# Kernel optimization log

Measured on AMD Instinct MI355X. Metric: run time of the kernel, lower is better.

## Reference

```python
import jax, jax.numpy as jnp
import numpy as np

B = 32768
IN_DIM = 768
HIDDENS = [2048, 1024, 512]
EMBED_DIM = 128
NUM_EMB = 1024
DEPTH = 3


def setup_inputs() -> dict:
    key = jax.random.key(0)
    ks = jax.random.split(key, 20)
    d = {"x": jax.random.normal(ks[0], (B, IN_DIM), dtype=jnp.float32)}
    # Encoder: in -> h0 -> h1 -> h2 -> embed  (weights stored as [in, out])
    enc_dims = [IN_DIM] + HIDDENS + [EMBED_DIM]
    for i in range(4):
        fan_in = enc_dims[i]
        d[f"enc_W{i+1}"] = jax.random.normal(ks[1 + i], (enc_dims[i], enc_dims[i + 1]), dtype=jnp.float32) / np.sqrt(fan_in)
        d[f"enc_b{i+1}"] = jnp.zeros((enc_dims[i + 1],), dtype=jnp.float32)
    # Decoder: embed -> h0 -> h1 -> h2 -> in
    dec_dims = [EMBED_DIM] + HIDDENS + [IN_DIM]
    for i in range(4):
        fan_in = dec_dims[i]
        d[f"dec_W{i+1}"] = jax.random.normal(ks[5 + i], (dec_dims[i], dec_dims[i + 1]), dtype=jnp.float32) / np.sqrt(fan_in)
        d[f"dec_b{i+1}"] = jnp.zeros((dec_dims[i + 1],), dtype=jnp.float32)
    # Codebook (nn.Embedding weight, initialized ~ N(0,1) as in the module)
    d["codebook"] = jax.random.normal(ks[9], (NUM_EMB, EMBED_DIM), dtype=jnp.float32)
    return d


def _encoder(x, W1, b1, W2, b2, W3, b3, W4, b4):
    x = jax.nn.relu(x @ W1 + b1)
    x = jax.nn.relu(x @ W2 + b2)
    x = jax.nn.relu(x @ W3 + b3)
    return x @ W4 + b4


def _decoder(x, W1, b1, W2, b2, W3, b3, W4, b4):
    x = jax.nn.relu(x @ W1 + b1)
    x = jax.nn.relu(x @ W2 + b2)
    x = jax.nn.relu(x @ W3 + b3)
    return x @ W4 + b4


def reference(x,
              enc_W1, enc_b1, enc_W2, enc_b2, enc_W3, enc_b3, enc_W4, enc_b4,
              dec_W1, dec_b1, dec_W2, dec_b2, dec_W3, dec_b3, dec_W4, dec_b4,
              codebook):
    z = _encoder(x, enc_W1, enc_b1, enc_W2, enc_b2, enc_W3, enc_b3, enc_W4, enc_b4)
    z_det = jax.lax.stop_gradient(z)

    cb_sq = jnp.sum(codebook * codebook, axis=1)  # [K]
    residue = z_det
    z_hat = jnp.zeros_like(z_det)
    codes = []
    for _ in range(DEPTH):  # residual quantization loop
        # squared L2 distances [B, K]
        dist = (jnp.sum(residue * residue, axis=1, keepdims=True)
                + cb_sq
                - 2.0 * residue @ codebook.T)
        idx = jnp.argmin(dist, axis=1)          # [B]
        codes.append(idx)
        z_hat = z_hat + codebook[idx]           # gather codebook vectors
        residue = z_det - z_hat
    all_codes = jnp.stack(codes, axis=1)        # [B, DEPTH] int

    # straight-through estimator: forward uses z_hat, grad flows through z
    z_flow = z + jax.lax.stop_gradient(z_hat - z)
    x_recon = _decoder(z_flow, dec_W1, dec_b1, dec_W2, dec_b2, dec_W3, dec_b3, dec_W4, dec_b4)
    return (x_recon, all_codes)
```

## Files before the change

kernel.cpp:

```cpp
#include <hip/hip_runtime.h>

#define FLT_MAX_C 3.402823466e+38f

typedef __attribute__((ext_vector_type(8))) __bf16 bf16x8;
typedef __attribute__((ext_vector_type(4))) float f32x4;

static __device__ __forceinline__ ushort f2bf(float x) {
    union { float f; unsigned u; } v; v.f = x;
    unsigned r = (v.u + 0x7FFFu + ((v.u >> 16) & 1u)) >> 16;
    return (ushort)r;
}

template<bool RELU>
__global__ __launch_bounds__(256) void gemm_f32(
    const float* __restrict__ A, const float* __restrict__ W,
    const float* __restrict__ bias, float* __restrict__ C,
    int M, int K, int N)
{
    __shared__ float As[8][128];
    __shared__ float Bs[8][132];
    const int tid = threadIdx.x;
    const int bm = blockIdx.y << 7;
    const int bn = blockIdx.x << 7;

    const int la_row = tid >> 1;
    const int la_k   = (tid & 1) << 2;
    const int lb_row = tid >> 5;
    const int lb_col = (tid & 31) << 2;
    const int tm4 = (tid >> 4) << 2;
    const int tn4 = (tid & 15) << 2;

    float acc[8][8];
    #pragma unroll
    for (int i = 0; i < 8; ++i)
        #pragma unroll
        for (int j = 0; j < 8; ++j) acc[i][j] = 0.f;

    const float* aptr = A + (size_t)(bm + la_row) * K + la_k;
    const float* bptr = W + (size_t)lb_row * N + bn + lb_col;

    float4 av = *(const float4*)(aptr);
    float4 bv = *(const float4*)(bptr);

    for (int k0 = 0; k0 < K; k0 += 8) {
        __syncthreads();
        As[la_k + 0][la_row] = av.x;
        As[la_k + 1][la_row] = av.y;
        As[la_k + 2][la_row] = av.z;
        As[la_k + 3][la_row] = av.w;
        *(float4*)(&Bs[lb_row][lb_col]) = bv;
        __syncthreads();
        if (k0 + 8 < K) {
            av = *(const float4*)(aptr + k0 + 8);
            bv = *(const float4*)(bptr + (size_t)(k0 + 8) * N);
        }
        #pragma unroll
        for (int kk = 0; kk < 8; ++kk) {
            float a[8], b[8];
            *(float4*)(a)     = *(const float4*)(&As[kk][tm4]);
            *(float4*)(a + 4) = *(const float4*)(&As[kk][tm4 + 64]);
            *(float4*)(b)     = *(const float4*)(&Bs[kk][tn4]);
            *(float4*)(b + 4) = *(const float4*)(&Bs[kk][tn4 + 64]);
            #pragma unroll
            for (int i = 0; i < 8; ++i)
                #pragma unroll
                for (int j = 0; j < 8; ++j)
                    acc[i][j] = fmaf(a[i], b[j], acc[i][j]);
        }
    }

    float bv0[8];
    #pragma unroll
    for (int j = 0; j < 8; ++j)
        bv0[j] = bias[bn + tn4 + (j < 4 ? j : 64 + j - 4)];

    #pragma unroll
    for (int i = 0; i < 8; ++i) {
        int row = bm + tm4 + (i < 4 ? i : 64 + i - 4);
        float* cp = C + (size_t)row * N + bn + tn4;
        float4 v0, v1;
        v0.x = acc[i][0] + bv0[0]; v0.y = acc[i][1] + bv0[1];
        v0.z = acc[i][2] + bv0[2]; v0.w = acc[i][3] + bv0[3];
        v1.x = acc[i][4] + bv0[4]; v1.y = acc[i][5] + bv0[5];
        v1.z = acc[i][6] + bv0[6]; v1.w = acc[i][7] + bv0[7];
        if (RELU) {
            v0.x = fmaxf(v0.x, 0.f); v0.y = fmaxf(v0.y, 0.f);
            v0.z = fmaxf(v0.z, 0.f); v0.w = fmaxf(v0.w, 0.f);
            v1.x = fmaxf(v1.x, 0.f); v1.y = fmaxf(v1.y, 0.f);
            v1.z = fmaxf(v1.z, 0.f); v1.w = fmaxf(v1.w, 0.f);
        }
        *(float4*)(cp) = v0;
        *(float4*)(cp + 64) = v1;
    }
}

template<bool RELU, bool OUTF32>
__global__ __launch_bounds__(256) void gemm_bf16(
    const ushort* __restrict__ A,
    const ushort* __restrict__ Wt,
    const float* __restrict__ bias,
    void* __restrict__ C,
    int M, int K, int N)
{
    __shared__ __align__(16) ushort As[128][64];
    __shared__ __align__(16) ushort Bs[128][64];
    const int tid  = threadIdx.x;
    const int lane = tid & 63;
    const int wv   = tid >> 6;
    const int wm   = (wv >> 1) << 6;
    const int wn   = (wv & 1) << 6;
    const int bm   = blockIdx.y << 7;
    const int bn   = blockIdx.x << 7;
    const int lr   = lane & 15;
    const int lh   = lane >> 4;

    f32x4 acc[4][4];
    #pragma unroll
    for (int m = 0; m < 4; ++m)
        #pragma unroll
        for (int n = 0; n < 4; ++n) acc[m][n] = (f32x4){0.f, 0.f, 0.f, 0.f};

    for (int k0 = 0; k0 < K; k0 += 64) {
        __syncthreads();
        #pragma unroll
        for (int i = 0; i < 4; ++i) {
            const int c    = wv * 4 + i;
            const int boff = c * 1024 + lane * 16;
            const int r    = boff >> 7;
            const int cb   = boff & 127;
            const char* sa = (const char*)A  + (((size_t)(bm + r) * K + k0) << 1) + cb;
            const char* sb = (const char*)Wt + (((size_t)(bn + r) * K + k0) << 1) + cb;
            __builtin_amdgcn_global_load_lds((const void*)sa, (void*)(&As[0][0] + c * 512), 16, 0, 0);
            __builtin_amdgcn_global_load_lds((const void*)sb, (void*)(&Bs[0][0] + c * 512), 16, 0, 0);
        }
        __syncthreads();
        #pragma unroll
        for (int kk = 0; kk < 64; kk += 32) {
            bf16x8 af[4], bfr[4];
            #pragma unroll
            for (int m = 0; m < 4; ++m)
                af[m] = *(const bf16x8*)&As[wm + m * 16 + lr][kk + lh * 8];
            #pragma unroll
            for (int n = 0; n < 4; ++n)
                bfr[n] = *(const bf16x8*)&Bs[wn + n * 16 + lr][kk + lh * 8];
            #pragma unroll
            for (int m = 0; m < 4; ++m)
                #pragma unroll
                for (int n = 0; n < 4; ++n)
                    acc[m][n] = __builtin_amdgcn_mfma_f32_16x16x32_bf16(
                        af[m], bfr[n], acc[m][n], 0, 0, 0);
        }
    }

    #pragma unroll
    for (int n = 0; n < 4; ++n) {
        const int col = bn + wn + n * 16 + lr;
        const float bcol = bias[col];
        #pragma unroll
        for (int m = 0; m < 4; ++m) {
            #pragma unroll
            for (int i = 0; i < 4; ++i) {
                const int row = bm + wm + m * 16 + lh * 4 + i;
                float v = acc[m][n][i] + bcol;
                if (RELU) v = fmaxf(v, 0.f);
                if (OUTF32) ((float*)C)[(size_t)row * N + col] = v;
                else        ((ushort*)C)[(size_t)row * N + col] = f2bf(v);
            }
        }
    }
}

__global__ __launch_bounds__(256) void wt_convert(
    const float* __restrict__ W, ushort* __restrict__ Wt, int K, int N)
{
    __shared__ ushort t[64][65];
    const int kb = blockIdx.y << 6, nb = blockIdx.x << 6;
    const int c  = threadIdx.x & 63;
    const int r0 = (threadIdx.x >> 6) << 4;
    #pragma unroll
    for (int i = 0; i < 16; ++i)
        t[r0 + i][c] = f2bf(W[(size_t)(kb + r0 + i) * N + nb + c]);
    __syncthreads();
    #pragma unroll
    for (int i = 0; i < 16; ++i)
        Wt[(size_t)(nb + r0 + i) * K + kb + c] = t[c][r0 + i];
}

__global__ __launch_bounds__(256) void cbsq_kernel(
    const float* __restrict__ cb, float* __restrict__ cbsq)
{
    int k = blockIdx.x * 256 + threadIdx.x;
    const float* r = cb + ((size_t)k << 7);
    float s = 0.f;
    #pragma unroll 8
    for (int d = 0; d < 128; ++d) s = fmaf(r[d], r[d], s);
    cbsq[k] = s;
}

__global__ __launch_bounds__(256) void quant_kernel(
    const float* __restrict__ z, const float* __restrict__ cb,
    const float* __restrict__ cbsq, ushort* __restrict__ zhat_bf,
    float* __restrict__ codes)
{
    __shared__ float rs[16][128];
    __shared__ float cbl[64][132];
    __shared__ float cbsq_l[1024];

    const int tid  = threadIdx.x;
    const int lane = tid & 63;
    const int wv   = tid >> 6;
    const int row0 = blockIdx.x << 4;

    #pragma unroll
    for (int i = 0; i < 2; ++i) {
        int f = tid + (i << 8);
        ((float4*)rs)[f] = ((const float4*)(z + ((size_t)row0 << 7)))[f];
    }
    #pragma unroll
    for (int i = 0; i < 4; ++i) cbsq_l[tid + (i << 8)] = cbsq[tid + (i << 8)];
    __syncthreads();

    for (int t = 0; t < 3; ++t) {
        float rr_[4];
        #pragma unroll
        for (int j = 0; j < 4; ++j) {
            const float* rp = rs[wv * 4 + j];
            float v0 = rp[lane * 2], v1 = rp[lane * 2 + 1];
            float p = v0 * v0 + v1 * v1;
            #pragma unroll
            for (int off = 32; off >= 1; off >>= 1) p += __shfl_xor(p, off);
            rr_[j] = p;
        }

        float best_d[4] = {FLT_MAX_C, FLT_MAX_C, FLT_MAX_C, FLT_MAX_C};
        int   best_i[4] = {0, 0, 0, 0};

        for (int c = 0; c < 16; ++c) {
            __syncthreads();
            #pragma unroll
            for (int i = 0; i < 8; ++i) {
                int f    = tid + (i << 8);
                int code = f >> 5;
                int d4   = f & 31;
                float4 v = ((const float4*)(cb + ((size_t)(c * 64 + code) << 7)))[d4];
                *(float4*)(&cbl[code][d4 << 2]) = v;
            }
            __syncthreads();

            const int k = c * 64 + lane;
            float acc0 = 0.f, acc1 = 0.f, acc2 = 0.f, acc3 = 0.f;
            #pragma unroll 8
            for (int d4 = 0; d4 < 32; ++d4) {
                float4 cv = *(const float4*)(&cbl[lane][d4 << 2]);
                float4 r0 = *(const float4*)(&rs[wv * 4 + 0][d4 << 2]);
                float4 r1 = *(const float4*)(&rs[wv * 4 + 1][d4 << 2]);
                float4 r2 = *(const float4*)(&rs[wv * 4 + 2][d4 << 2]);
                float4 r3 = *(const float4*)(&rs[wv * 4 + 3][d4 << 2]);
                acc0 = fmaf(r0.x, cv.x, acc0); acc0 = fmaf(r0.y, cv.y, acc0);
                acc0 = fmaf(r0.z, cv.z, acc0); acc0 = fmaf(r0.w, cv.w, acc0);
                acc1 = fmaf(r1.x, cv.x, acc1); acc1 = fmaf(r1.y, cv.y, acc1);
                acc1 = fmaf(r1.z, cv.z, acc1); acc1 = fmaf(r1.w, cv.w, acc1);
                acc2 = fmaf(r2.x, cv.x, acc2); acc2 = fmaf(r2.y, cv.y, acc2);
                acc2 = fmaf(r2.z, cv.z, acc2); acc2 = fmaf(r2.w, cv.w, acc2);
                acc3 = fmaf(r3.x, cv.x, acc3); acc3 = fmaf(r3.y, cv.y, acc3);
                acc3 = fmaf(r3.z, cv.z, acc3); acc3 = fmaf(r3.w, cv.w, acc3);
            }
            float dd[4];
            dd[0] = (rr_[0] + cbsq_l[k]) - 2.f * acc0;
            dd[1] = (rr_[1] + cbsq_l[k]) - 2.f * acc1;
            dd[2] = (rr_[2] + cbsq_l[k]) - 2.f * acc2;
            dd[3] = (rr_[3] + cbsq_l[k]) - 2.f * acc3;
            #pragma unroll
            for (int j = 0; j < 4; ++j)
                if (dd[j] < best_d[j]) { best_d[j] = dd[j]; best_i[j] = k; }
        }

        #pragma unroll
        for (int j = 0; j < 4; ++j) {
            float d = best_d[j]; int bi = best_i[j];
            #pragma unroll
            for (int off = 32; off >= 1; off >>= 1) {
                float od = __shfl_xor(d, off);
                int   oi = __shfl_xor(bi, off);
                if (od < d || (od == d && oi < bi)) { d = od; bi = oi; }
            }
            best_d[j] = d; best_i[j] = bi;
        }

        #pragma unroll
        for (int j = 0; j < 4; ++j) {
            int row = row0 + wv * 4 + j;
            if (lane == 0) codes[(size_t)row * 3 + t] = (float)best_i[j];
            const float* cvec = cb + ((size_t)best_i[j] << 7);
            rs[wv * 4 + j][lane * 2]     -= cvec[lane * 2];
            rs[wv * 4 + j][lane * 2 + 1] -= cvec[lane * 2 + 1];
        }
    }

    __syncthreads();
    #pragma unroll
    for (int i = 0; i < 2; ++i) {
        int f = tid + (i << 8);
        float4 zv = ((const float4*)(z + ((size_t)row0 << 7)))[f];
        float4 rv = ((float4*)rs)[f];
        ushort4 o;
        o.x = f2bf(zv.x - rv.x); o.y = f2bf(zv.y - rv.y);
        o.z = f2bf(zv.z - rv.z); o.w = f2bf(zv.w - rv.w);
        ((ushort4*)(zhat_bf + ((size_t)row0 << 7)))[f] = o;
    }
}

extern "C" void kernel_launch(void* const* d_in, const int* in_sizes, int n_in,
                              void* d_out, int out_size, void* d_ws, size_t ws_size,
                              hipStream_t stream)
{
    const float* x   = (const float*)d_in[0];
    const float* eW1 = (const float*)d_in[1];
    const float* eb1 = (const float*)d_in[2];
    const float* eW2 = (const float*)d_in[3];
    const float* eb2 = (const float*)d_in[4];
    const float* eW3 = (const float*)d_in[5];
    const float* eb3 = (const float*)d_in[6];
    const float* eW4 = (const float*)d_in[7];
    const float* eb4 = (const float*)d_in[8];
    const float* dW1 = (const float*)d_in[9];
    const float* db1 = (const float*)d_in[10];
    const float* dW2 = (const float*)d_in[11];
    const float* db2 = (const float*)d_in[12];
    const float* dW3 = (const float*)d_in[13];
    const float* db3 = (const float*)d_in[14];
    const float* dW4 = (const float*)d_in[15];
    const float* db4 = (const float*)d_in[16];
    const float* cb  = (const float*)d_in[17];

    float* out   = (float*)d_out;
    float* codes = out + (size_t)32768 * 768;

    ushort* Wt1 = (ushort*)d_ws;
    ushort* Wt2 = Wt1 + (size_t)2048 * 128;
    ushort* Wt3 = Wt2 + (size_t)1024 * 2048;
    ushort* Wt4 = Wt3 + (size_t)512 * 1024;
    float*  sq  = (float*)(Wt4 + (size_t)768 * 512);
    float*  act = sq + 1024;
    const size_t fixed_b = (char*)act - (char*)d_ws;

    int mc = 32768;
    while (mc > 1024) {
        if (fixed_b + (size_t)mc * 15104 <= ws_size) break;
        mc >>= 1;
    }

    float*  R1  = act;
    float*  R2  = R1 + (size_t)mc * 2048;
    float*  R3  = R2 + (size_t)mc * 1024;
    float*  RZ  = R3 + (size_t)mc * 512;
    ushort* ZHb = (ushort*)(RZ + (size_t)mc * 128);
    ushort* D1  = (ushort*)R1;
    ushort* D2  = (ushort*)R2;
    ushort* D3  = (ushort*)R3;

    wt_convert<<<dim3(2048 / 64, 128 / 64), 256, 0, stream>>>(dW1, Wt1, 128, 2048);
    wt_convert<<<dim3(1024 / 64, 2048 / 64), 256, 0, stream>>>(dW2, Wt2, 2048, 1024);
    wt_convert<<<dim3(512 / 64, 1024 / 64), 256, 0, stream>>>(dW3, Wt3, 1024, 512);
    wt_convert<<<dim3(768 / 64, 512 / 64), 256, 0, stream>>>(dW4, Wt4, 512, 768);
    cbsq_kernel<<<4, 256, 0, stream>>>(cb, sq);

    const int mg = mc >> 7;
    for (int r0 = 0; r0 < 32768; r0 += mc) {
        const float* xi     = x     + (size_t)r0 * 768;
        float*       outi   = out   + (size_t)r0 * 768;
        float*       codesi = codes + (size_t)r0 * 3;
        gemm_f32<true ><<<dim3(16, mg), 256, 0, stream>>>(xi, eW1, eb1, R1, mc, 768,  2048);
        gemm_f32<true ><<<dim3( 8, mg), 256, 0, stream>>>(R1, eW2, eb2, R2, mc, 2048, 1024);
        gemm_f32<true ><<<dim3( 4, mg), 256, 0, stream>>>(R2, eW3, eb3, R3, mc, 1024, 512);
        gemm_f32<false><<<dim3( 1, mg), 256, 0, stream>>>(R3, eW4, eb4, RZ, mc, 512,  128);
        quant_kernel<<<mc >> 4, 256, 0, stream>>>(RZ, cb, sq, ZHb, codesi);
        gemm_bf16<true , false><<<dim3(16, mg), 256, 0, stream>>>(ZHb, Wt1, db1, D1,   mc, 128,  2048);
        gemm_bf16<true , false><<<dim3( 8, mg), 256, 0, stream>>>(D1,  Wt2, db2, D2,   mc, 2048, 1024);
        gemm_bf16<true , false><<<dim3( 4, mg), 256, 0, stream>>>(D2,  Wt3, db3, D3,   mc, 1024, 512);
        gemm_bf16<false, true ><<<dim3( 6, mg), 256, 0, stream>>>(D3,  Wt4, db4, outi, mc, 512,  768);
    }
}
```

Measured before the change: 4.348 ms.

## Widen fp32 encoder GEMM tiles and restructure quantizer to row-per-thread registers

The fp32 encoder GEMMs now use a 128x256 output tile (16 accumulators per thread) with launch bounds asking for two blocks per SM, which raises arithmetic intensity per shared-memory load. The quantizer is rewritten so each thread holds a full 128-wide residual row in registers. Each wave scans a quarter of the codebook directly from global/cache memory, and the partial minima are merged through shared memory. This removes the shared-memory codebook staging and the per-chunk syncs, at the cost of heavy register pressure (128 floats of residual plus 64 accumulators) and possible spills or lower occupancy.

New measurement: 7.019 ms. 61.4% more time.

```diff
diff --git a/kernel.cpp b/kernel.cpp
--- a/kernel.cpp
+++ b/kernel.cpp
@@ -11,36 +11,44 @@
     return (ushort)r;
 }
 
-template<bool RELU>
-__global__ __launch_bounds__(256) void gemm_f32(
+template<bool RELU, int BN, int TAG>
+__global__ __launch_bounds__(256, 2) void gemm_f32(
     const float* __restrict__ A, const float* __restrict__ W,
     const float* __restrict__ bias, float* __restrict__ C,
     int M, int K, int N)
 {
+    constexpr int NQ  = BN / 64;
+    constexpr int NC  = NQ * 4;
+    constexpr int BF4 = BN / 4;
+    constexpr int BI  = (8 * BF4) / 256;
+
     __shared__ float As[8][128];
-    __shared__ float Bs[8][132];
+    __shared__ float Bs[8][BN + 4];
     const int tid = threadIdx.x;
     const int bm = blockIdx.y << 7;
-    const int bn = blockIdx.x << 7;
+    const int bn = blockIdx.x * BN;
 
     const int la_row = tid >> 1;
     const int la_k   = (tid & 1) << 2;
-    const int lb_row = tid >> 5;
-    const int lb_col = (tid & 31) << 2;
     const int tm4 = (tid >> 4) << 2;
     const int tn4 = (tid & 15) << 2;
 
-    float acc[8][8];
+    float acc[8][NC];
     #pragma unroll
     for (int i = 0; i < 8; ++i)
         #pragma unroll
-        for (int j = 0; j < 8; ++j) acc[i][j] = 0.f;
+        for (int j = 0; j < NC; ++j) acc[i][j] = 0.f;
 
     const float* aptr = A + (size_t)(bm + la_row) * K + la_k;
-    const float* bptr = W + (size_t)lb_row * N + bn + lb_col;
 
     float4 av = *(const float4*)(aptr);
-    float4 bv = *(const float4*)(bptr);
+    float4 bv[BI];
+    #pragma unroll
+    for (int i = 0; i < BI; ++i) {
+        int f = tid + (i << 8);
+        int row = f / BF4, col4 = f % BF4;
+        bv[i] = *(const float4*)(W + (size_t)row * N + bn + col4 * 4);
+    }
 
     for (int k0 = 0; k0 < K; k0 += 8) {
         __syncthreads();
@@ -48,53 +56,66 @@
         As[la_k + 1][la_row] = av.y;
         As[la_k + 2][la_row] = av.z;
         As[la_k + 3][la_row] = av.w;
-        *(float4*)(&Bs[lb_row][lb_col]) = bv;
+        #pragma unroll
+        for (int i = 0; i < BI; ++i) {
+            int f = tid + (i << 8);
+            int row = f / BF4, col4 = f % BF4;
+            *(float4*)(&Bs[row][col4 * 4]) = bv[i];
+        }
         __syncthreads();
         if (k0 + 8 < K) {
             av = *(const float4*)(aptr + k0 + 8);
-            bv = *(const float4*)(bptr + (size_t)(k0 + 8) * N);
+            #pragma unroll
+            for (int i = 0; i < BI; ++i) {
+                int f = tid + (i << 8);
+                int row = f / BF4, col4 = f % BF4;
+                bv[i] = *(const float4*)(W + (size_t)(k0 + 8 + row) * N + bn + col4 * 4);
+            }
         }
         #pragma unroll
         for (int kk = 0; kk < 8; ++kk) {
-            float a[8], b[8];
+            float a[8], b[NC];
             *(float4*)(a)     = *(const float4*)(&As[kk][tm4]);
             *(float4*)(a + 4) = *(const float4*)(&As[kk][tm4 + 64]);
-            *(float4*)(b)     = *(const float4*)(&Bs[kk][tn4]);
-            *(float4*)(b + 4) = *(const float4*)(&Bs[kk][tn4 + 64]);
+            #pragma unroll
+            for (int q = 0; q < NQ; ++q)
+                *(float4*)(b + q * 4) = *(const float4*)(&Bs[kk][tn4 + 64 * q]);
             #pragma unroll
             for (int i = 0; i < 8; ++i)
                 #pragma unroll
-                for (int j = 0; j < 8; ++j)
+                for (int j = 0; j < NC; ++j)
                     acc[i][j] = fmaf(a[i], b[j], acc[i][j]);
         }
     }
 
-    float bv0[8];
-    #pragma unroll
-    for (int j = 0; j < 8; ++j)
-        bv0[j] = bias[bn + tn4 + (j < 4 ? j : 64 + j - 4)];
+    float bb[NC];
+    #pragma unroll
+    for (int q = 0; q < NQ; ++q)
+        #pragma unroll
+        for (int jj = 0; jj < 4; ++jj)
+            bb[q * 4 + jj] = bias[bn + tn4 + 64 * q + jj];
 
     #pragma unroll
     for (int i = 0; i < 8; ++i) {
-        int row = bm + tm4 + (i < 4 ? i : 64 + i - 4);
+        int row = bm + tm4 + (i < 4 ? i : 60 + i);
         float* cp = C + (size_t)row * N + bn + tn4;
-        float4 v0, v1;
-        v0.x = acc[i][0] + bv0[0]; v0.y = acc[i][1] + bv0[1];
-        v0.z = acc[i][2] + bv0[2]; v0.w = acc[i][3] + bv0[3];
-        v1.x = acc[i][4] + bv0[4]; v1.y = acc[i][5] + bv0[5];
-        v1.z = acc[i][6] + bv0[6]; v1.w = acc[i][7] + bv0[7];
-        if (RELU) {
-            v0.x = fmaxf(v0.x, 0.f); v0.y = fmaxf(v0.y, 0.f);
-            v0.z = fmaxf(v0.z, 0.f); v0.w = fmaxf(v0.w, 0.f);
-            v1.x = fmaxf(v1.x, 0.f); v1.y = fmaxf(v1.y, 0.f);
-            v1.z = fmaxf(v1.z, 0.f); v1.w = fmaxf(v1.w, 0.f);
-        }
-        *(float4*)(cp) = v0;
-        *(float4*)(cp + 64) = v1;
-    }
-}
-
-template<bool RELU, bool OUTF32>
+        #pragma unroll
+        for (int q = 0; q < NQ; ++q) {
+            float4 v;
+            v.x = acc[i][q * 4 + 0] + bb[q * 4 + 0];
+            v.y = acc[i][q * 4 + 1] + bb[q * 4 + 1];
+            v.z = acc[i][q * 4 + 2] + bb[q * 4 + 2];
+            v.w = acc[i][q * 4 + 3] + bb[q * 4 + 3];
+            if (RELU) {
+                v.x = fmaxf(v.x, 0.f); v.y = fmaxf(v.y, 0.f);
+                v.z = fmaxf(v.z, 0.f); v.w = fmaxf(v.w, 0.f);
+            }
+            *(float4*)(cp + 64 * q) = v;
+        }
+    }
+}
+
+template<bool RELU, bool OUTF32, int TAG>
 __global__ __launch_bounds__(256) void gemm_bf16(
     const ushort* __restrict__ A,
     const ushort* __restrict__ Wt,
@@ -197,116 +218,80 @@
     cbsq[k] = s;
 }
 
-__global__ __launch_bounds__(256) void quant_kernel(
+__global__ __launch_bounds__(256, 2) void quant_kernel(
     const float* __restrict__ z, const float* __restrict__ cb,
     const float* __restrict__ cbsq, ushort* __restrict__ zhat_bf,
     float* __restrict__ codes)
 {
-    __shared__ float rs[16][128];
-    __shared__ float cbl[64][132];
-    __shared__ float cbsq_l[1024];
-
-    const int tid  = threadIdx.x;
-    const int lane = tid & 63;
-    const int wv   = tid >> 6;
-    const int row0 = blockIdx.x << 4;
-
-    #pragma unroll
-    for (int i = 0; i < 2; ++i) {
-        int f = tid + (i << 8);
-        ((float4*)rs)[f] = ((const float4*)(z + ((size_t)row0 << 7)))[f];
-    }
-    #pragma unroll
-    for (int i = 0; i < 4; ++i) cbsq_l[tid + (i << 8)] = cbsq[tid + (i << 8)];
-    __syncthreads();
+    __shared__ float sd[4][64];
+    __shared__ int   si[4][64];
+
+    const int lane = threadIdx.x & 63;
+    const int wv   = threadIdx.x >> 6;
+    const size_t row = (size_t)blockIdx.x * 64 + lane;
+
+    const float4* zr = (const float4*)(z + row * 128);
+    float4 r[32];
+    #pragma unroll
+    for (int i = 0; i < 32; ++i) r[i] = zr[i];
 
     for (int t = 0; t < 3; ++t) {
-        float rr_[4];
-        #pragma unroll
-        for (int j = 0; j < 4; ++j) {
-            const float* rp = rs[wv * 4 + j];
-            float v0 = rp[lane * 2], v1 = rp[lane * 2 + 1];
-            float p = v0 * v0 + v1 * v1;
-            #pragma unroll
-            for (int off = 32; off >= 1; off >>= 1) p += __shfl_xor(p, off);
-            rr_[j] = p;
-        }
-
-        float best_d[4] = {FLT_MAX_C, FLT_MAX_C, FLT_MAX_C, FLT_MAX_C};
-        int   best_i[4] = {0, 0, 0, 0};
-
-        for (int c = 0; c < 16; ++c) {
-            __syncthreads();
-            #pragma unroll
-            for (int i = 0; i < 8; ++i) {
-                int f    = tid + (i << 8);
-                int code = f >> 5;
-                int d4   = f & 31;
-                float4 v = ((const float4*)(cb + ((size_t)(c * 64 + code) << 7)))[d4];
-                *(float4*)(&cbl[code][d4 << 2]) = v;
+        float4 rr4 = {0.f, 0.f, 0.f, 0.f};
+        #pragma unroll
+        for (int i = 0; i < 32; ++i) {
+            rr4.x = fmaf(r[i].x, r[i].x, rr4.x);
+            rr4.y = fmaf(r[i].y, r[i].y, rr4.y);
+            rr4.z = fmaf(r[i].z, r[i].z, rr4.z);
+            rr4.w = fmaf(r[i].w, r[i].w, rr4.w);
+        }
+        const float rr = (rr4.x + rr4.y) + (rr4.z + rr4.w);
+
+        float bd = FLT_MAX_C; int bi = 0;
+        const int kbeg = wv << 8;
+        for (int k = kbeg; k < kbeg + 256; ++k) {
+            const float4* c4 = (const float4*)(cb + ((size_t)k << 7));
+            float4 a4 = {0.f, 0.f, 0.f, 0.f};
+            #pragma unroll
+            for (int i = 0; i < 32; ++i) {
+                float4 cv = c4[i];
+                a4.x = fmaf(r[i].x, cv.x, a4.x);
+                a4.y = fmaf(r[i].y, cv.y, a4.y);
+                a4.z = fmaf(r[i].z, cv.z, a4.z);
+                a4.w = fmaf(r[i].w, cv.w, a4.w);
             }
-            __syncthreads();
-
-            const int k = c * 64 + lane;
-            float acc0 = 0.f, acc1 = 0.f, acc2 = 0.f, acc3 = 0.f;
-            #pragma unroll 8
-            for (int d4 = 0; d4 < 32; ++d4) {
-                float4 cv = *(const float4*)(&cbl[lane][d4 << 2]);
-                float4 r0 = *(const float4*)(&rs[wv * 4 + 0][d4 << 2]);
-                float4 r1 = *(const float4*)(&rs[wv * 4 + 1][d4 << 2]);
-                float4 r2 = *(const float4*)(&rs[wv * 4 + 2][d4 << 2]);
-                float4 r3 = *(const float4*)(&rs[wv * 4 + 3][d4 << 2]);
-                acc0 = fmaf(r0.x, cv.x, acc0); acc0 = fmaf(r0.y, cv.y, acc0);
-                acc0 = fmaf(r0.z, cv.z, acc0); acc0 = fmaf(r0.w, cv.w, acc0);
-                acc1 = fmaf(r1.x, cv.x, acc1); acc1 = fmaf(r1.y, cv.y, acc1);
-                acc1 = fmaf(r1.z, cv.z, acc1); acc1 = fmaf(r1.w, cv.w, acc1);
-                acc2 = fmaf(r2.x, cv.x, acc2); acc2 = fmaf(r2.y, cv.y, acc2);
-                acc2 = fmaf(r2.z, cv.z, acc2); acc2 = fmaf(r2.w, cv.w, acc2);
-                acc3 = fmaf(r3.x, cv.x, acc3); acc3 = fmaf(r3.y, cv.y, acc3);
-                acc3 = fmaf(r3.z, cv.z, acc3); acc3 = fmaf(r3.w, cv.w, acc3);
-            }
-            float dd[4];
-            dd[0] = (rr_[0] + cbsq_l[k]) - 2.f * acc0;
-            dd[1] = (rr_[1] + cbsq_l[k]) - 2.f * acc1;
-            dd[2] = (rr_[2] + cbsq_l[k]) - 2.f * acc2;
-            dd[3] = (rr_[3] + cbsq_l[k]) - 2.f * acc3;
-            #pragma unroll
-            for (int j = 0; j < 4; ++j)
-                if (dd[j] < best_d[j]) { best_d[j] = dd[j]; best_i[j] = k; }
-        }
-
-        #pragma unroll
-        for (int j = 0; j < 4; ++j) {
-            float d = best_d[j]; int bi = best_i[j];
-            #pragma unroll
-            for (int off = 32; off >= 1; off >>= 1) {
-                float od = __shfl_xor(d, off);
-                int   oi = __shfl_xor(bi, off);
-                if (od < d || (od == d && oi < bi)) { d = od; bi = oi; }
-            }
-            best_d[j] = d; best_i[j] = bi;
-        }
-
-        #pragma unroll
-        for (int j = 0; j < 4; ++j) {
-            int row = row0 + wv * 4 + j;
-            if (lane == 0) codes[(size_t)row * 3 + t] = (float)best_i[j];
-            const float* cvec = cb + ((size_t)best_i[j] << 7);
-            rs[wv * 4 + j][lane * 2]     -= cvec[lane * 2];
-            rs[wv * 4 + j][lane * 2 + 1] -= cvec[lane * 2 + 1];
-        }
-    }
-
-    __syncthreads();
-    #pragma unroll
-    for (int i = 0; i < 2; ++i) {
-        int f = tid + (i << 8);
-        float4 zv = ((const float4*)(z + ((size_t)row0 << 7)))[f];
-        float4 rv = ((float4*)rs)[f];
+            float dot  = (a4.x + a4.y) + (a4.z + a4.w);
+            float dist = (rr + cbsq[k]) - 2.f * dot;
+            if (dist < bd) { bd = dist; bi = k; }
+        }
+        sd[wv][lane] = bd; si[wv][lane] = bi;
+        __syncthreads();
+        float d = sd[0][lane]; int bidx = si[0][lane];
+        #pragma unroll
+        for (int w = 1; w < 4; ++w) {
+            float dw = sd[w][lane]; int iw = si[w][lane];
+            if (dw < d) { d = dw; bidx = iw; }
+        }
+        __syncthreads();
+
+        if (wv == 0) codes[row * 3 + t] = (float)bidx;
+
+        const float4* cbest = (const float4*)(cb + ((size_t)bidx << 7));
+        #pragma unroll
+        for (int i = 0; i < 32; ++i) {
+            float4 cv = cbest[i];
+            r[i].x -= cv.x; r[i].y -= cv.y; r[i].z -= cv.z; r[i].w -= cv.w;
+        }
+    }
+
+    ushort* zrow = zhat_bf + row * 128;
+    #pragma unroll
+    for (int i = 0; i < 8; ++i) {
+        const int idx = (wv << 3) + i;
+        float4 zv = zr[idx];
         ushort4 o;
-        o.x = f2bf(zv.x - rv.x); o.y = f2bf(zv.y - rv.y);
-        o.z = f2bf(zv.z - rv.z); o.w = f2bf(zv.w - rv.w);
-        ((ushort4*)(zhat_bf + ((size_t)row0 << 7)))[f] = o;
+        o.x = f2bf(zv.x - r[idx].x); o.y = f2bf(zv.y - r[idx].y);
+        o.z = f2bf(zv.z - r[idx].z); o.w = f2bf(zv.w - r[idx].w);
+        ((ushort4*)zrow)[idx] = o;
     }
 }
 
@@ -370,14 +355,14 @@
         const float* xi     = x     + (size_t)r0 * 768;
         float*       outi   = out   + (size_t)r0 * 768;
         float*       codesi = codes + (size_t)r0 * 3;
-        gemm_f32<true ><<<dim3(16, mg), 256, 0, stream>>>(xi, eW1, eb1, R1, mc, 768,  2048);
-        gemm_f32<true ><<<dim3( 8, mg), 256, 0, stream>>>(R1, eW2, eb2, R2, mc, 2048, 1024);
-        gemm_f32<true ><<<dim3( 4, mg), 256, 0, stream>>>(R2, eW3, eb3, R3, mc, 1024, 512);
-        gemm_f32<false><<<dim3( 1, mg), 256, 0, stream>>>(R3, eW4, eb4, RZ, mc, 512,  128);
-        quant_kernel<<<mc >> 4, 256, 0, stream>>>(RZ, cb, sq, ZHb, codesi);
-        gemm_bf16<true , false><<<dim3(16, mg), 256, 0, stream>>>(ZHb, Wt1, db1, D1,   mc, 128,  2048);
-        gemm_bf16<true , false><<<dim3( 8, mg), 256, 0, stream>>>(D1,  Wt2, db2, D2,   mc, 2048, 1024);
-        gemm_bf16<true , false><<<dim3( 4, mg), 256, 0, stream>>>(D2,  Wt3, db3, D3,   mc, 1024, 512);
-        gemm_bf16<false, true ><<<dim3( 6, mg), 256, 0, stream>>>(D3,  Wt4, db4, outi, mc, 512,  768);
-    }
-}
+        gemm_f32<true , 256, 1><<<dim3( 8, mg), 256, 0, stream>>>(xi, eW1, eb1, R1, mc, 768,  2048);
+        gemm_f32<true , 256, 2><<<dim3( 4, mg), 256, 0, stream>>>(R1, eW2, eb2, R2, mc, 2048, 1024);
+        gemm_f32<true , 256, 3><<<dim3( 2, mg), 256, 0, stream>>>(R2, eW3, eb3, R3, mc, 1024, 512);
+        gemm_f32<false, 128, 4><<<dim3( 1, mg), 256, 0, stream>>>(R3, eW4, eb4, RZ, mc, 512,  128);
+        quant_kernel<<<mc >> 6, 256, 0, stream>>>(RZ, cb, sq, ZHb, codesi);
+        gemm_bf16<true , false, 5><<<dim3(16, mg), 256, 0, stream>>>(ZHb, Wt1, db1, D1,   mc, 128,  2048);
+        gemm_bf16<true , false, 6><<<dim3( 8, mg), 256, 0, stream>>>(D1,  Wt2, db2, D2,   mc, 2048, 1024);
+        gemm_bf16<true , false, 7><<<dim3( 4, mg), 256, 0, stream>>>(D2,  Wt3, db3, D3,   mc, 1024, 512);
+        gemm_bf16<false, true , 8><<<dim3( 6, mg), 256, 0, stream>>>(D3,  Wt4, db4, outi, mc, 512,  768);
+    }
+}
```
